# Kernel optimization log

Hardware: AMD Instinct MI355X
Metric: run time of the kernel (lower is better)

The kernel has to match this reference:

```python
import jax, jax.numpy as jnp
import numpy as np

GROUPS = 32
N_HEADS = 16
EPS = 1e-5


def setup_inputs() -> dict:
    key = jax.random.key(0)
    ks = jax.random.split(key, 5)
    b, c, t = 4, 1024, 1024
    return {
        "x": jax.random.normal(ks[0], (b, c, t), dtype=jnp.float32),
        "gn_weight": jnp.ones((c,), dtype=jnp.float32),
        "gn_bias": jnp.zeros((c,), dtype=jnp.float32),
        "qkv_w": jax.random.normal(ks[1], (3 * c, c), dtype=jnp.float32) * (c ** -0.5),
        "qkv_b": jax.random.normal(ks[2], (3 * c,), dtype=jnp.float32) * 0.02,
        "proj_w": jax.random.normal(ks[3], (c, c), dtype=jnp.float32) * (c ** -0.5),
        "proj_b": jax.random.normal(ks[4], (c,), dtype=jnp.float32) * 0.02,
    }


def _group_norm(x, weight, bias):
    # x: [b, c, t]; GroupNorm32 computes stats in float32 (already fp32 here)
    b, c, t = x.shape
    xg = x.reshape(b, GROUPS, c // GROUPS, t)
    mean = xg.mean(axis=(2, 3), keepdims=True)
    var = xg.var(axis=(2, 3), keepdims=True)
    xn = ((xg - mean) * jax.lax.rsqrt(var + EPS)).reshape(b, c, t)
    return xn * weight[None, :, None] + bias[None, :, None]


def reference(x, gn_weight, gn_bias, qkv_w, qkv_b, proj_w, proj_b):
    b, c, t = x.shape
    xn = _group_norm(x, gn_weight, gn_bias)
    # 1x1 Conv1d == channel matmul: [3c, c] x [b, c, t] -> [b, 3c, t]
    qkv = jnp.einsum('oc,bct->bot', qkv_w, xn) + qkv_b[None, :, None]
    ch = c // N_HEADS
    # legacy per-head interleaved layout: reshape to [b*H, 3*ch, t], split
    qkv = qkv.reshape(b * N_HEADS, 3 * ch, t)
    q, k, v = qkv[:, :ch], qkv[:, ch:2 * ch], qkv[:, 2 * ch:]
    scale = ch ** -0.25  # 1/sqrt(sqrt(ch)), applied to both q and k
    weight = jnp.einsum('bct,bcs->bts', q * scale, k * scale)  # [b*H, t, t]
    weight = jax.nn.softmax(weight.astype(jnp.float32), axis=-1).astype(weight.dtype)
    a = jnp.einsum('bts,bcs->bct', weight, v).reshape(b, c, t)
    h = jnp.einsum('oc,bct->bot', proj_w, a) + proj_b[None, :, None]
    return x + h
```

## Files before the change

### kernel.cpp

```cpp
#include <hip/hip_runtime.h>
#include <hip/hip_bf16.h>

typedef __bf16 bf16;
typedef __bf16 bf16x2 __attribute__((ext_vector_type(2)));
typedef __bf16 bf16x4 __attribute__((ext_vector_type(4)));
typedef __bf16 bf16x8 __attribute__((ext_vector_type(8)));
typedef float  f32x4  __attribute__((ext_vector_type(4)));

static __device__ __forceinline__ f32x4 mfma16(bf16x8 a, bf16x8 b, f32x4 c) {
  return __builtin_amdgcn_mfma_f32_16x16x32_bf16(a, b, c, 0, 0, 0);
}

static __device__ __forceinline__ void gload_lds16(const bf16* g, bf16* l) {
  __builtin_amdgcn_global_load_lds(
      (const __attribute__((address_space(1))) void*)g,
      (__attribute__((address_space(3))) void*)l, 16, 0, 0);
}

#define VMCNT0() asm volatile("s_waitcnt vmcnt(0)" ::: "memory")
#define VMCNT4() asm volatile("s_waitcnt vmcnt(4)" ::: "memory")
#define BARRIER()                                        \
  do {                                                   \
    asm volatile("" ::: "memory");                       \
    __builtin_amdgcn_s_barrier();                        \
    asm volatile("" ::: "memory");                       \
  } while (0)

__global__ __launch_bounds__(256) void cvt2_kernel(const float* __restrict__ wa,
                                                   bf16* __restrict__ oa,
                                                   const float* __restrict__ wb,
                                                   bf16* __restrict__ ob) {
  int i = blockIdx.x * 256 + threadIdx.x;
  const int na4 = 3072 * 1024 / 4;
  const float* src; bf16* dst;
  if (i < na4) { src = wa; dst = oa; }
  else         { src = wb; dst = ob; i -= na4; }
  float4 v = ((const float4*)src)[i];
  bf16x4 o = { (bf16)v.x, (bf16)v.y, (bf16)v.z, (bf16)v.w };
  *(bf16x4*)(dst + 4ll * i) = o;
}

__global__ __launch_bounds__(512) void gn_kernel(const float* __restrict__ x,
                                                 const float* __restrict__ w,
                                                 const float* __restrict__ bias,
                                                 bf16* __restrict__ xnT) {
  int id = blockIdx.x;
  int b = id >> 7, g = (id >> 2) & 31, qtr = id & 3;
  const float* xb = x + ((size_t)b * 1024 + g * 32) * 1024;
  int tid = threadIdx.x;
  float s = 0.f, sq = 0.f;
  const float4* x4 = (const float4*)xb;
  for (int i = tid; i < 8192; i += 512) {
    float4 v = x4[i];
    s  += v.x + v.y + v.z + v.w;
    sq += v.x * v.x + v.y * v.y + v.z * v.z + v.w * v.w;
  }
#pragma unroll
  for (int off = 32; off; off >>= 1) { s += __shfl_down(s, off); sq += __shfl_down(sq, off); }
  __shared__ float red[16];
  int wv = tid >> 6;
  if ((tid & 63) == 0) { red[wv] = s; red[8 + wv] = sq; }
  __syncthreads();
  s = 0.f; sq = 0.f;
#pragma unroll
  for (int i = 0; i < 8; ++i) { s += red[i]; sq += red[8 + i]; }
  float mean = s * (1.f / 32768.f);
  float var  = sq * (1.f / 32768.f) - mean * mean;
  float rstd = rsqrtf(var + 1e-5f);

  __shared__ bf16 tile[64][36];
  int c = tid >> 4, q = tid & 15;
  int r = tid >> 3, q2 = tid & 7;
  float wc = w[g * 32 + c] * rstd;
  float fb = bias[g * 32 + c] - mean * wc;
  for (int t0 = qtr * 256; t0 < qtr * 256 + 256; t0 += 64) {
    float4 v = *(const float4*)(xb + (size_t)c * 1024 + t0 + q * 4);
    tile[q * 4 + 0][c] = (bf16)(v.x * wc + fb);
    tile[q * 4 + 1][c] = (bf16)(v.y * wc + fb);
    tile[q * 4 + 2][c] = (bf16)(v.z * wc + fb);
    tile[q * 4 + 3][c] = (bf16)(v.w * wc + fb);
    __syncthreads();
    *(bf16x4*)&xnT[((size_t)b * 1024 + t0 + r) * 1024 + g * 32 + q2 * 4] =
        *(bf16x4*)&tile[r][q2 * 4];
    __syncthreads();
  }
}

__global__ __launch_bounds__(512, 1) void qkv_kernel(
    const bf16* __restrict__ A, const bf16* __restrict__ Bw,
    const float* __restrict__ bias,
    bf16* __restrict__ qkT, bf16* __restrict__ vC) {
  extern __shared__ __align__(16) bf16 smem[];

  int tid = threadIdx.x, wid = tid >> 6, lane = tid & 63;
  int l15 = lane & 15, l4 = lane >> 4;
  int wr = wid >> 2, wc = wid & 3;
  int rsw = (l15 & 7) << 4;

  int sid = (blockIdx.x & 7) * 32 + (blockIdx.x >> 3);
  int bx = sid & 15, by = (sid >> 4) & 3, z = sid >> 6;
  int m0 = by * 256, n0 = bx * 192;
  const bf16* Ab = A + (size_t)z * 1024 * 1024 + (size_t)m0 * 1024;
  const bf16* Bb = Bw + (size_t)n0 * 1024;

  int srow = tid >> 3;
  int csw  = (tid & 7) ^ (srow & 7);
  auto stageA = [&](int d, int kt) {
    bf16* dst = smem + d * 16384;
    const bf16* src = Ab + kt * 64 + csw * 8;
#pragma unroll
    for (int hh = 0; hh < 2; ++hh)
#pragma unroll
      for (int L = 0; L < 2; ++L)
        gload_lds16(src + (size_t)(hh * 128 + L * 64 + srow) * 1024,
                    dst + hh * 8192 + (L * 512 + wid * 64) * 8);
  };
  auto stageB = [&](int d, int kt) {
    bf16* dst = smem + 49152 + d * 12288;
    const bf16* src = Bb + kt * 64 + csw * 8;
#pragma unroll
    for (int L = 0; L < 3; ++L)
      gload_lds16(src + (size_t)(L * 64 + srow) * 1024, dst + (L * 512 + wid * 64) * 8);
  };

  f32x4 acc[8][3] = {};

  auto compute = [&](int ta, int tb) {
    const char* Ab8 = (const char*)smem + ta * 32768 + wr * 16384;
    const char* Bb8 = (const char*)smem + 98304 + tb * 24576;
    bf16x8 bfr[3][2], af[4][2];
#pragma unroll
    for (int ni = 0; ni < 3; ++ni) {
      int rb = (wc * 48 + ni * 16 + l15) * 128;
#pragma unroll
      for (int kk = 0; kk < 2; ++kk)
        bfr[ni][kk] = *(const bf16x8*)(Bb8 + rb + ((kk * 64 + l4 * 16) ^ rsw));
    }
#pragma unroll
    for (int mi = 0; mi < 4; ++mi) {
      int rb = (mi * 16 + l15) * 128;
#pragma unroll
      for (int kk = 0; kk < 2; ++kk)
        af[mi][kk] = *(const bf16x8*)(Ab8 + rb + ((kk * 64 + l4 * 16) ^ rsw));
    }
#pragma unroll
    for (int mi = 0; mi < 4; ++mi)
#pragma unroll
      for (int ni = 0; ni < 3; ++ni)
#pragma unroll
        for (int kk = 0; kk < 2; ++kk)
          acc[mi][ni] = mfma16(af[mi][kk], bfr[ni][kk], acc[mi][ni]);
#pragma unroll
    for (int mi = 0; mi < 4; ++mi) {
      int rb = ((4 + mi) * 16 + l15) * 128;
#pragma unroll
      for (int kk = 0; kk < 2; ++kk)
        af[mi][kk] = *(const bf16x8*)(Ab8 + rb + ((kk * 64 + l4 * 16) ^ rsw));
    }
#pragma unroll
    for (int mi = 0; mi < 4; ++mi)
#pragma unroll
      for (int ni = 0; ni < 3; ++ni)
#pragma unroll
        for (int kk = 0; kk < 2; ++kk)
          acc[4 + mi][ni] = mfma16(af[mi][kk], bfr[ni][kk], acc[4 + mi][ni]);
  };

  stageA(0, 0); stageB(0, 0); stageA(1, 1);
  VMCNT4();
  BARRIER();

  for (int t = 0; t < 14; ++t) {
    stageB((t + 1) & 1, t + 1);
    stageA((t + 2) % 3, t + 2);
    compute(t % 3, t & 1);
    VMCNT4();
    BARRIER();
  }
  stageB(1, 15);
  compute(2, 0);
  VMCNT0();
  BARRIER();
  compute(0, 1);

  const float scale = 0.35355339059327373f;
  int h = bx;
#pragma unroll
  for (int ni = 0; ni < 3; ++ni) {
    int oin = wc * 48 + ni * 16;
    float bv = bias[n0 + oin + l15];
#pragma unroll
    for (int mi = 0; mi < 8; ++mi) {
      int tb = m0 + wr * 128 + mi * 16 + l4 * 4;
      f32x4 v = acc[mi][ni];
      if (oin < 128) {
#pragma unroll
        for (int i = 0; i < 4; ++i)
          qkT[((size_t)z * 1024 + tb + i) * 2048 + h * 128 + oin + l15] =
              (bf16)((v[i] + bv) * scale);
      } else {
        bf16x4 st = { (bf16)(v[0] + bv), (bf16)(v[1] + bv),
                      (bf16)(v[2] + bv), (bf16)(v[3] + bv) };
        *(bf16x4*)&vC[(((size_t)z * 16 + h) * 64 + (oin - 128 + l15)) * 1024 + tb] = st;
      }
    }
  }
}

template <int MODE>
__global__ __launch_bounds__(256) void gemm_kernel(
    const bf16* __restrict__ A, const bf16* __restrict__ Bw,
    const float* __restrict__ bias,
    bf16* __restrict__ qkT, bf16* __restrict__ vC,
    const float* __restrict__ xres, float* __restrict__ out) {
  __shared__ bf16 At[128 * 32];
  __shared__ bf16 Bt[128 * 32];
  int tid = threadIdx.x;
  int wid = tid >> 6, lane = tid & 63;
  int l15 = lane & 15, l4 = lane >> 4;
  int wm = wid >> 1, wn = wid & 1;
  int z = blockIdx.z;
  int m0 = blockIdx.y * 128, n0 = blockIdx.x * 128;
  const bf16* Ab = A + (size_t)z * 1024 * 1024 + (size_t)m0 * 1024;
  const bf16* Bb = Bw + (size_t)n0 * 1024;

  f32x4 acc[4][4] = {};

  for (int k0 = 0; k0 < 1024; k0 += 32) {
#pragma unroll
    for (int j = 0; j < 2; ++j) {
      int slot = j * 256 + tid;
      int row  = slot >> 2;
      int ck   = (slot & 3) ^ ((row >> 1) & 3);
      gload_lds16(Ab + (size_t)row * 1024 + k0 + ck * 8, At + (size_t)(j * 256 + wid * 64) * 8);
      gload_lds16(Bb + (size_t)row * 1024 + k0 + ck * 8, Bt + (size_t)(j * 256 + wid * 64) * 8);
    }
    __syncthreads();
    bf16x8 af[4], bfr[4];
#pragma unroll
    for (int mi = 0; mi < 4; ++mi) {
      int row = wm * 64 + mi * 16 + l15;
      int ck  = l4 ^ ((row >> 1) & 3);
      af[mi] = *(const bf16x8*)(At + row * 32 + ck * 8);
    }
#pragma unroll
    for (int nf = 0; nf < 4; ++nf) {
      int row = wn * 64 + nf * 16 + l15;
      int ck  = l4 ^ ((row >> 1) & 3);
      bfr[nf] = *(const bf16x8*)(Bt + row * 32 + ck * 8);
    }
#pragma unroll
    for (int mi = 0; mi < 4; ++mi)
#pragma unroll
      for (int nf = 0; nf < 4; ++nf)
        acc[mi][nf] = mfma16(af[mi], bfr[nf], acc[mi][nf]);
    __syncthreads();
  }

  if (MODE == 1) {
#pragma unroll
    for (int nf = 0; nf < 4; ++nf) {
      int o = n0 + wn * 64 + nf * 16 + l15;
      float bv = bias[o];
#pragma unroll
      for (int mi = 0; mi < 4; ++mi) {
        int tb = m0 + wm * 64 + mi * 16 + l4 * 4;
        size_t base = ((size_t)z * 1024 + o) * 1024 + tb;
        float4 xr = *(const float4*)(xres + base);
        f32x4 v = acc[mi][nf];
        float4 ov = { xr.x + v[0] + bv, xr.y + v[1] + bv,
                      xr.z + v[2] + bv, xr.w + v[3] + bv };
        *(float4*)(out + base) = ov;
      }
    }
  }
}

__global__ __launch_bounds__(512, 4) void attn_kernel(const bf16* __restrict__ qkT,
                                                      const bf16* __restrict__ vC,
                                                      bf16* __restrict__ aT) {
  __shared__ __align__(16) bf16 Kt[2][64 * 64];
  __shared__ __align__(16) bf16 Vt[2][64 * 64];
  __shared__ __align__(16) bf16 Pt[8][16 * 64];

  int id = blockIdx.x;
  int sid = (id & 7) * 64 + (id >> 3);
  int head = sid >> 3, tblk = sid & 7;
  int b = head >> 4, h = head & 15;
  int t0 = tblk * 128;
  int tid = threadIdx.x, wid = tid >> 6, lane = tid & 63;
  int l15 = lane & 15, l4 = lane >> 4;
  int trow = t0 + wid * 16;

  const bf16* kbase = qkT + (size_t)b * 1024 * 2048 + h * 128 + 64;
  const bf16* vbase = vC + (size_t)(b * 16 + h) * 64 * 1024;
  char* Pw = (char*)Pt[wid];
  int rsw = (l15 & 7) << 4;
  char* PwRow = Pw + l15 * 128;

  const bf16* qrow = qkT + ((size_t)b * 1024 + trow + l15) * 2048 + h * 128;
  bf16x8 qf[2];
#pragma unroll
  for (int kb = 0; kb < 2; ++kb) qf[kb] = *(const bf16x8*)(qrow + kb * 32 + l4 * 8);

  int rl = lane >> 3;
  int scol = (((lane & 7) * 16) ^ (rl << 4)) >> 1;
  int r8 = wid * 8 + rl;
  auto stage = [&](int buf, int st) {
    int s0 = st * 64;
    gload_lds16(kbase + (size_t)(s0 + r8) * 2048 + scol, &Kt[buf][wid * 512]);
    gload_lds16(vbase + (size_t)r8 * 1024 + s0 + scol, &Vt[buf][wid * 512]);
  };

  float m_run = -1e30f, l_run = 0.f;
  f32x4 oacc[4] = {};

  stage(0, 0);
  __syncthreads();

  for (int st = 0; st < 16; ++st) {
    int cur = st & 1;
    if (st < 15) stage(cur ^ 1, st + 1);

    const char* Kb = (const char*)Kt[cur];
    f32x4 sf[4];
#pragma unroll
    for (int nf = 0; nf < 4; ++nf) sf[nf] = (f32x4){0.f, 0.f, 0.f, 0.f};
    __builtin_amdgcn_s_setprio(1);
#pragma unroll
    for (int nf = 0; nf < 4; ++nf) {
      int rr = nf * 16 + l15;
#pragma unroll
      for (int kb = 0; kb < 2; ++kb) {
        bf16x8 kf = *(const bf16x8*)(Kb + rr * 128 + ((kb * 64 + l4 * 16) ^ rsw));
        sf[nf] = mfma16(kf, qf[kb], sf[nf]);
      }
    }
    __builtin_amdgcn_s_setprio(0);

    float mb;
    {
      float a0 = fmaxf(fmaxf(sf[0][0], sf[0][1]), fmaxf(sf[0][2], sf[0][3]));
      float a1 = fmaxf(fmaxf(sf[1][0], sf[1][1]), fmaxf(sf[1][2], sf[1][3]));
      float a2 = fmaxf(fmaxf(sf[2][0], sf[2][1]), fmaxf(sf[2][2], sf[2][3]));
      float a3 = fmaxf(fmaxf(sf[3][0], sf[3][1]), fmaxf(sf[3][2], sf[3][3]));
      mb = fmaxf(fmaxf(a0, a1), fmaxf(a2, a3));
    }
    mb = fmaxf(mb, __shfl_xor(mb, 16));
    mb = fmaxf(mb, __shfl_xor(mb, 32));
    if (!__all(mb - m_run <= 8.f)) {
      float mn = fmaxf(m_run, mb);
      float corr = __expf(m_run - mn);
      m_run = mn;
      l_run *= corr;
#pragma unroll
      for (int cf = 0; cf < 4; ++cf)
#pragma unroll
        for (int i = 0; i < 4; ++i) oacc[cf][i] *= corr;
    }
    float sb = 0.f;
#pragma unroll
    for (int nf = 0; nf < 4; ++nf) {
      float p0 = __expf(sf[nf][0] - m_run), p1 = __expf(sf[nf][1] - m_run);
      float p2 = __expf(sf[nf][2] - m_run), p3 = __expf(sf[nf][3] - m_run);
      sb += (p0 + p1) + (p2 + p3);
      int off = nf * 32 + l4 * 8;
      *(bf16x4*)(PwRow + (off ^ rsw)) = (bf16x4){ (bf16)p0, (bf16)p1, (bf16)p2, (bf16)p3 };
    }
    sb += __shfl_xor(sb, 16);
    sb += __shfl_xor(sb, 32);
    l_run += sb;

    const char* Vb = (const char*)Vt[cur];
    __builtin_amdgcn_s_setprio(1);
#pragma unroll
    for (int kb = 0; kb < 2; ++kb) {
      bf16x8 pf = *(const bf16x8*)(Pw + l15 * 128 + ((kb * 64 + l4 * 16) ^ rsw));
#pragma unroll
      for (int cf = 0; cf < 4; ++cf) {
        int rr = cf * 16 + l15;
        bf16x8 vf = *(const bf16x8*)(Vb + rr * 128 + ((kb * 64 + l4 * 16) ^ rsw));
        oacc[cf] = mfma16(vf, pf, oacc[cf]);
      }
    }
    __builtin_amdgcn_s_setprio(0);
    __syncthreads();
  }

  float rdiv = 1.f / l_run;
  int t = trow + l15;
#pragma unroll
  for (int cf = 0; cf < 4; ++cf) {
    bf16x4 ov = { (bf16)(oacc[cf][0] * rdiv), (bf16)(oacc[cf][1] * rdiv),
                  (bf16)(oacc[cf][2] * rdiv), (bf16)(oacc[cf][3] * rdiv) };
    *(bf16x4*)&aT[((size_t)b * 1024 + t) * 1024 + h * 64 + cf * 16 + l4 * 4] = ov;
  }
}

extern "C" void kernel_launch(void* const* d_in, const int* in_sizes, int n_in,
                              void* d_out, int out_size, void* d_ws, size_t ws_size,
                              hipStream_t stream) {
  const float* x      = (const float*)d_in[0];
  const float* gw     = (const float*)d_in[1];
  const float* gb     = (const float*)d_in[2];
  const float* qkv_w  = (const float*)d_in[3];
  const float* qkv_b  = (const float*)d_in[4];
  const float* proj_w = (const float*)d_in[5];
  const float* proj_b = (const float*)d_in[6];
  float* out = (float*)d_out;

  char* ws = (char*)d_ws;
  bf16* wq_bf = (bf16*)(ws);
  bf16* wp_bf = (bf16*)(ws + 6ll  * 1024 * 1024);
  bf16* xnT   = (bf16*)(ws + 8ll  * 1024 * 1024);
  bf16* qkT   = (bf16*)(ws + 16ll * 1024 * 1024);
  bf16* vC    = (bf16*)(ws + 32ll * 1024 * 1024);
  bf16* aT    = (bf16*)(ws + 40ll * 1024 * 1024);

  hipFuncSetAttribute(reinterpret_cast<const void*>(qkv_kernel),
                      hipFuncAttributeMaxDynamicSharedMemorySize, 147456);

  cvt2_kernel<<<dim3(4096), dim3(256), 0, stream>>>(qkv_w, wq_bf, proj_w, wp_bf);
  gn_kernel<<<dim3(512), dim3(512), 0, stream>>>(x, gw, gb, xnT);
  qkv_kernel<<<dim3(256), dim3(512), 147456, stream>>>(xnT, wq_bf, qkv_b, qkT, vC);
  attn_kernel<<<dim3(512), dim3(512), 0, stream>>>(qkT, vC, aT);
  gemm_kernel<1><<<dim3(8, 8, 4), dim3(256), 0, stream>>>(aT, wp_bf, proj_b, nullptr, nullptr, x, out);
}
```

Before: 107.1 us.

## Fuse weight conversion into group-norm kernel and pipeline projection GEMM

Merges the weight fp32-to-bf16 conversion and the group-norm kernels into one launch, using extra blocks for the conversion work, which saves a launch and lets the two jobs run concurrently. Replaces the simple synchronous projection GEMM with a 512-thread kernel that uses dynamic LDS, K-tiles of 64, triple-buffered A and double-buffered B staging with partial vmcnt waits, XOR-swizzled LDS, and a remapped block order. This is meant to hide global load latency behind MFMA work, at the cost of more LDS per block and lower occupancy (launch bounds of 1 block per CU).

```diff
diff --git a/kernel.cpp b/kernel.cpp
--- a/kernel.cpp
+++ b/kernel.cpp
@@ -18,6 +18,7 @@
 }
 
 #define VMCNT0() asm volatile("s_waitcnt vmcnt(0)" ::: "memory")
+#define VMCNT2() asm volatile("s_waitcnt vmcnt(2)" ::: "memory")
 #define VMCNT4() asm volatile("s_waitcnt vmcnt(4)" ::: "memory")
 #define BARRIER()                                        \
   do {                                                   \
@@ -26,28 +27,30 @@
     asm volatile("" ::: "memory");                       \
   } while (0)
 
-__global__ __launch_bounds__(256) void cvt2_kernel(const float* __restrict__ wa,
-                                                   bf16* __restrict__ oa,
-                                                   const float* __restrict__ wb,
-                                                   bf16* __restrict__ ob) {
-  int i = blockIdx.x * 256 + threadIdx.x;
-  const int na4 = 3072 * 1024 / 4;
-  const float* src; bf16* dst;
-  if (i < na4) { src = wa; dst = oa; }
-  else         { src = wb; dst = ob; i -= na4; }
-  float4 v = ((const float4*)src)[i];
-  bf16x4 o = { (bf16)v.x, (bf16)v.y, (bf16)v.z, (bf16)v.w };
-  *(bf16x4*)(dst + 4ll * i) = o;
-}
-
-__global__ __launch_bounds__(512) void gn_kernel(const float* __restrict__ x,
-                                                 const float* __restrict__ w,
-                                                 const float* __restrict__ bias,
-                                                 bf16* __restrict__ xnT) {
-  int id = blockIdx.x;
+__global__ __launch_bounds__(512) void pre_kernel(const float* __restrict__ x,
+                                                  const float* __restrict__ gw,
+                                                  const float* __restrict__ gb,
+                                                  bf16* __restrict__ xnT,
+                                                  const float* __restrict__ qkv_w,
+                                                  bf16* __restrict__ wq,
+                                                  const float* __restrict__ proj_w,
+                                                  bf16* __restrict__ wp) {
+  int blk = blockIdx.x;
+  int tid = threadIdx.x;
+  if (blk >= 512) {
+    int i = (blk - 512) * 512 + tid;
+    const int na4 = 3072 * 1024 / 4;
+    const float* src; bf16* dst;
+    if (i < na4) { src = qkv_w; dst = wq; }
+    else         { src = proj_w; dst = wp; i -= na4; }
+    float4 v = ((const float4*)src)[i];
+    bf16x4 o = { (bf16)v.x, (bf16)v.y, (bf16)v.z, (bf16)v.w };
+    *(bf16x4*)(dst + 4ll * i) = o;
+    return;
+  }
+  int id = blk;
   int b = id >> 7, g = (id >> 2) & 31, qtr = id & 3;
   const float* xb = x + ((size_t)b * 1024 + g * 32) * 1024;
-  int tid = threadIdx.x;
   float s = 0.f, sq = 0.f;
   const float4* x4 = (const float4*)xb;
   for (int i = tid; i < 8192; i += 512) {
@@ -71,8 +74,8 @@
   __shared__ bf16 tile[64][36];
   int c = tid >> 4, q = tid & 15;
   int r = tid >> 3, q2 = tid & 7;
-  float wc = w[g * 32 + c] * rstd;
-  float fb = bias[g * 32 + c] - mean * wc;
+  float wc = gw[g * 32 + c] * rstd;
+  float fb = gb[g * 32 + c] - mean * wc;
   for (int t0 = qtr * 256; t0 < qtr * 256 + 256; t0 += 64) {
     float4 v = *(const float4*)(xb + (size_t)c * 1024 + t0 + q * 4);
     tile[q * 4 + 0][c] = (bf16)(v.x * wc + fb);
@@ -207,71 +210,99 @@
   }
 }
 
-template <int MODE>
-__global__ __launch_bounds__(256) void gemm_kernel(
+__global__ __launch_bounds__(512, 1) void proj_kernel(
     const bf16* __restrict__ A, const bf16* __restrict__ Bw,
     const float* __restrict__ bias,
-    bf16* __restrict__ qkT, bf16* __restrict__ vC,
     const float* __restrict__ xres, float* __restrict__ out) {
-  __shared__ bf16 At[128 * 32];
-  __shared__ bf16 Bt[128 * 32];
-  int tid = threadIdx.x;
-  int wid = tid >> 6, lane = tid & 63;
+  extern __shared__ __align__(16) bf16 smem[];
+
+  int tid = threadIdx.x, wid = tid >> 6, lane = tid & 63;
   int l15 = lane & 15, l4 = lane >> 4;
-  int wm = wid >> 1, wn = wid & 1;
-  int z = blockIdx.z;
-  int m0 = blockIdx.y * 128, n0 = blockIdx.x * 128;
+  int wr = wid >> 2, wc = wid & 3;
+  int rsw = (l15 & 7) << 4;
+
+  int sid = (blockIdx.x & 7) * 32 + (blockIdx.x >> 3);
+  int bx = sid & 7, by = (sid >> 3) & 7, z = sid >> 6;
+  int m0 = by * 128, n0 = bx * 128;
   const bf16* Ab = A + (size_t)z * 1024 * 1024 + (size_t)m0 * 1024;
   const bf16* Bb = Bw + (size_t)n0 * 1024;
 
-  f32x4 acc[4][4] = {};
-
-  for (int k0 = 0; k0 < 1024; k0 += 32) {
-#pragma unroll
-    for (int j = 0; j < 2; ++j) {
-      int slot = j * 256 + tid;
-      int row  = slot >> 2;
-      int ck   = (slot & 3) ^ ((row >> 1) & 3);
-      gload_lds16(Ab + (size_t)row * 1024 + k0 + ck * 8, At + (size_t)(j * 256 + wid * 64) * 8);
-      gload_lds16(Bb + (size_t)row * 1024 + k0 + ck * 8, Bt + (size_t)(j * 256 + wid * 64) * 8);
-    }
-    __syncthreads();
-    bf16x8 af[4], bfr[4];
+  int srow = tid >> 3;
+  int csw  = (tid & 7) ^ (srow & 7);
+  auto stageA = [&](int d, int kt) {
+    bf16* dst = smem + d * 8192;
+    const bf16* src = Ab + kt * 64 + csw * 8;
+#pragma unroll
+    for (int L = 0; L < 2; ++L)
+      gload_lds16(src + (size_t)(L * 64 + srow) * 1024, dst + (L * 512 + wid * 64) * 8);
+  };
+  auto stageB = [&](int d, int kt) {
+    bf16* dst = smem + 24576 + d * 8192;
+    const bf16* src = Bb + kt * 64 + csw * 8;
+#pragma unroll
+    for (int L = 0; L < 2; ++L)
+      gload_lds16(src + (size_t)(L * 64 + srow) * 1024, dst + (L * 512 + wid * 64) * 8);
+  };
+
+  f32x4 acc[4][2] = {};
+
+  auto compute = [&](int ta, int tb) {
+    const char* Ab8 = (const char*)smem + ta * 16384 + wr * 8192;
+    const char* Bb8 = (const char*)smem + 49152 + tb * 16384;
+    bf16x8 bfr[2][2], af[4][2];
+#pragma unroll
+    for (int ni = 0; ni < 2; ++ni) {
+      int rb = (wc * 32 + ni * 16 + l15) * 128;
+#pragma unroll
+      for (int kk = 0; kk < 2; ++kk)
+        bfr[ni][kk] = *(const bf16x8*)(Bb8 + rb + ((kk * 64 + l4 * 16) ^ rsw));
+    }
 #pragma unroll
     for (int mi = 0; mi < 4; ++mi) {
-      int row = wm * 64 + mi * 16 + l15;
-      int ck  = l4 ^ ((row >> 1) & 3);
-      af[mi] = *(const bf16x8*)(At + row * 32 + ck * 8);
-    }
-#pragma unroll
-    for (int nf = 0; nf < 4; ++nf) {
-      int row = wn * 64 + nf * 16 + l15;
-      int ck  = l4 ^ ((row >> 1) & 3);
-      bfr[nf] = *(const bf16x8*)(Bt + row * 32 + ck * 8);
+      int rb = (mi * 16 + l15) * 128;
+#pragma unroll
+      for (int kk = 0; kk < 2; ++kk)
+        af[mi][kk] = *(const bf16x8*)(Ab8 + rb + ((kk * 64 + l4 * 16) ^ rsw));
     }
 #pragma unroll
     for (int mi = 0; mi < 4; ++mi)
 #pragma unroll
-      for (int nf = 0; nf < 4; ++nf)
-        acc[mi][nf] = mfma16(af[mi], bfr[nf], acc[mi][nf]);
-    __syncthreads();
-  }
-
-  if (MODE == 1) {
-#pragma unroll
-    for (int nf = 0; nf < 4; ++nf) {
-      int o = n0 + wn * 64 + nf * 16 + l15;
-      float bv = bias[o];
-#pragma unroll
-      for (int mi = 0; mi < 4; ++mi) {
-        int tb = m0 + wm * 64 + mi * 16 + l4 * 4;
-        size_t base = ((size_t)z * 1024 + o) * 1024 + tb;
-        float4 xr = *(const float4*)(xres + base);
-        f32x4 v = acc[mi][nf];
-        float4 ov = { xr.x + v[0] + bv, xr.y + v[1] + bv,
-                      xr.z + v[2] + bv, xr.w + v[3] + bv };
-        *(float4*)(out + base) = ov;
-      }
+      for (int ni = 0; ni < 2; ++ni)
+#pragma unroll
+        for (int kk = 0; kk < 2; ++kk)
+          acc[mi][ni] = mfma16(af[mi][kk], bfr[ni][kk], acc[mi][ni]);
+  };
+
+  stageA(0, 0); stageB(0, 0); stageA(1, 1);
+  VMCNT2();
+  BARRIER();
+
+  for (int t = 0; t < 14; ++t) {
+    stageB((t + 1) & 1, t + 1);
+    stageA((t + 2) % 3, t + 2);
+    compute(t % 3, t & 1);
+    VMCNT2();
+    BARRIER();
+  }
+  stageB(1, 15);
+  compute(2, 0);
+  VMCNT0();
+  BARRIER();
+  compute(0, 1);
+
+#pragma unroll
+  for (int ni = 0; ni < 2; ++ni) {
+    int o = n0 + wc * 32 + ni * 16 + l15;
+    float bv = bias[o];
+#pragma unroll
+    for (int mi = 0; mi < 4; ++mi) {
+      int tb = m0 + wr * 64 + mi * 16 + l4 * 4;
+      size_t base = ((size_t)z * 1024 + o) * 1024 + tb;
+      float4 xr = *(const float4*)(xres + base);
+      f32x4 v = acc[mi][ni];
+      float4 ov = { xr.x + v[0] + bv, xr.y + v[1] + bv,
+                    xr.z + v[2] + bv, xr.w + v[3] + bv };
+      *(float4*)(out + base) = ov;
     }
   }
 }
@@ -419,10 +450,11 @@
 
   hipFuncSetAttribute(reinterpret_cast<const void*>(qkv_kernel),
                       hipFuncAttributeMaxDynamicSharedMemorySize, 147456);
-
-  cvt2_kernel<<<dim3(4096), dim3(256), 0, stream>>>(qkv_w, wq_bf, proj_w, wp_bf);
-  gn_kernel<<<dim3(512), dim3(512), 0, stream>>>(x, gw, gb, xnT);
+  hipFuncSetAttribute(reinterpret_cast<const void*>(proj_kernel),
+                      hipFuncAttributeMaxDynamicSharedMemorySize, 81920);
+
+  pre_kernel<<<dim3(2560), dim3(512), 0, stream>>>(x, gw, gb, xnT, qkv_w, wq_bf, proj_w, wp_bf);
   qkv_kernel<<<dim3(256), dim3(512), 147456, stream>>>(xnT, wq_bf, qkv_b, qkT, vC);
   attn_kernel<<<dim3(512), dim3(512), 0, stream>>>(qkT, vC, aT);
-  gemm_kernel<1><<<dim3(8, 8, 4), dim3(256), 0, stream>>>(aT, wp_bf, proj_b, nullptr, nullptr, x, out);
-}
+  proj_kernel<<<dim3(256), dim3(512), 81920, stream>>>(aT, wp_bf, proj_b, x, out);
+}
```

Measured after the change: 96.33 us. -10.0%, faster.
